# Kernel tuning notes

Hardware: AMD Instinct MI355X
Metric: run time of the kernel (lower is better)

The kernel has to match this reference:

```python
import jax, jax.numpy as jnp
import numpy as np

B, L, D_MODEL, D_STATE, D_CONV, EXPAND = 2, 1024, 1024, 16, 4, 2
D_INNER = D_MODEL * EXPAND


def setup_inputs() -> dict:
    key = jax.random.key(0)
    ks = jax.random.split(key, 8)
    s = lambda fan: 1.0 / np.sqrt(fan)
    x = jax.random.normal(ks[0], (B, L, D_MODEL), jnp.float32)
    in_proj_w = jax.random.normal(ks[1], (D_MODEL, 2 * D_INNER), jnp.float32) * s(D_MODEL)
    conv_w = jax.random.normal(ks[2], (D_INNER, 1, D_CONV), jnp.float32) * s(D_CONV)
    conv_b = jax.random.normal(ks[3], (D_INNER,), jnp.float32) * 0.01
    x_proj_w = jax.random.normal(ks[4], (D_INNER, 2 * D_STATE + D_INNER), jnp.float32) * s(D_INNER)
    dt_proj_w = jax.random.normal(ks[5], (D_INNER, D_INNER), jnp.float32) * s(D_INNER)
    dt_proj_b = jax.random.normal(ks[6], (D_INNER,), jnp.float32) * 0.01
    A_log = jnp.log(jnp.tile(jnp.arange(1, D_STATE + 1, dtype=jnp.float32)[None, :], (D_INNER, 1)))
    D = jnp.ones((D_INNER,), jnp.float32)
    out_proj_w = jax.random.normal(ks[7], (D_INNER, D_MODEL), jnp.float32) * s(D_INNER)
    return {"x": x, "in_proj_w": in_proj_w, "conv_w": conv_w, "conv_b": conv_b,
            "x_proj_w": x_proj_w, "dt_proj_w": dt_proj_w, "dt_proj_b": dt_proj_b,
            "A_log": A_log, "D": D, "out_proj_w": out_proj_w}


def _mamba_forward(x, in_proj_w, conv_w, conv_b, x_proj_w, dt_proj_w, dt_proj_b, A_log, D, out_proj_w):
    Bb, Ll, _ = x.shape
    d_inner, _, d_conv = conv_w.shape
    d_state = A_log.shape[1]
    # input projection and gate split
    xz = x @ in_proj_w                       # [B, L, 2*Di]
    x_inner, z = jnp.split(xz, 2, axis=-1)   # each [B, L, Di]
    # causal depthwise conv (left pad k-1, truncate to L == torch pad+slice)
    xc = jnp.transpose(x_inner, (0, 2, 1))   # [B, Di, L]
    xc = jax.lax.conv_general_dilated(
        xc, conv_w, window_strides=(1,), padding=[(d_conv - 1, 0)],
        dimension_numbers=("NCH", "OIH", "NCH"), feature_group_count=d_inner)
    xc = xc + conv_b[None, :, None]
    u = jax.nn.silu(jnp.transpose(xc, (0, 2, 1)))  # [B, L, Di]
    # SSM parameter projections
    ssm = u @ x_proj_w                        # [B, L, 2N+Di]
    B_ssm = ssm[..., :d_state]                # [B, L, N]
    C_ssm = ssm[..., d_state:2 * d_state]     # [B, L, N]
    dt = jax.nn.softplus(ssm[..., 2 * d_state:] @ dt_proj_w + dt_proj_b)  # [B, L, Di]
    A_real = -jnp.exp(A_log)                  # [Di, N]
    # selective scan over sequence (recurrence via lax.scan)
    def step(h, inp):
        dt_t, B_t, u_t = inp                  # [B,Di], [B,N], [B,Di]
        dA = jnp.exp(dt_t[..., None] * A_real)            # [B, Di, N]
        dBu = dt_t[..., None] * B_t[:, None, :] * u_t[..., None]
        h = dA * h + dBu
        return h, h
    h0 = jnp.zeros((Bb, d_inner, d_state), x.dtype)
    xs = (jnp.swapaxes(dt, 0, 1), jnp.swapaxes(B_ssm, 0, 1), jnp.swapaxes(u, 0, 1))
    _, states = jax.lax.scan(step, h0, xs)    # [L, B, Di, N]
    y = jnp.einsum("lbdn,lbn->lbd", states, jnp.swapaxes(C_ssm, 0, 1))
    y = jnp.swapaxes(y, 0, 1) + D * u         # skip connection
    y = y * jax.nn.silu(z)                    # gating
    return y @ out_proj_w                     # [B, L, d_model]


def reference(x, in_proj_w, conv_w, conv_b, x_proj_w, dt_proj_w, dt_proj_b, A_log, D, out_proj_w):
    return _mamba_forward(x, in_proj_w, conv_w, conv_b, x_proj_w, dt_proj_w, dt_proj_b, A_log, D, out_proj_w)
```

## Files before the change

kernel.cpp:

```cpp
#include <hip/hip_runtime.h>
#include <hip/hip_bf16.h>

#define BB 2
#define LL 1024
#define DMODEL 1024
#define DINNER 2048
#define DSTATE 16
#define DCONV 4
#define MM (BB * LL)
#define N_XZ 4096
#define N_SSM 2080
#define N_SSM_PAD 2176
#define CCH 32
#define LCH 32

typedef __hip_bfloat16 bf16;
typedef short bf16x8 __attribute__((ext_vector_type(8)));
typedef float f32x4 __attribute__((ext_vector_type(4)));

__device__ __forceinline__ void load16_lds(const bf16* g, bf16* l) {
    __builtin_amdgcn_global_load_lds(
        (const __attribute__((address_space(1))) void*)g,
        (__attribute__((address_space(3))) void*)l,
        16, 0, 0);
}

__global__ __launch_bounds__(256) void prep_kernel(
    const float* __restrict__ x, bf16* __restrict__ xbf,
    const float* __restrict__ w1, bf16* __restrict__ o1,
    const float* __restrict__ w2, bf16* __restrict__ o2,
    const float* __restrict__ w3, bf16* __restrict__ o3,
    const float* __restrict__ w4, bf16* __restrict__ o4)
{
    int bid = blockIdx.x;
    const float* src; bf16* dst; int K, N, tn, tk;
    if (bid < 4096)        { src = w1; dst = o1; K = 1024; N = 4096; tn = bid & 127; tk = bid >> 7; }
    else if (bid < 8256)   { bid -= 4096;  src = w2; dst = o2; K = 2048; N = 2080; tn = bid % 65; tk = bid / 65; }
    else if (bid < 12352)  { bid -= 8256;  src = w3; dst = o3; K = 2048; N = 2048; tn = bid & 63; tk = bid >> 6; }
    else if (bid < 14400)  { bid -= 12352; src = w4; dst = o4; K = 2048; N = 1024; tn = bid & 31; tk = bid >> 5; }
    else {
        bid -= 14400;
        int i = (bid * 256 + threadIdx.x) * 4;
        float4 v = *(const float4*)(x + i);
        xbf[i + 0] = __float2bfloat16(v.x);
        xbf[i + 1] = __float2bfloat16(v.y);
        xbf[i + 2] = __float2bfloat16(v.z);
        xbf[i + 3] = __float2bfloat16(v.w);
        return;
    }
    __shared__ float tile[32][33];
    const int nb = tn * 32, kb = tk * 32;
    const int tx = threadIdx.x & 31, ty = threadIdx.x >> 5;
    #pragma unroll
    for (int i = 0; i < 32; i += 8) {
        int k = kb + ty + i, n = nb + tx;
        tile[ty + i][tx] = (k < K && n < N) ? src[(size_t)k * N + n] : 0.f;
    }
    __syncthreads();
    #pragma unroll
    for (int i = 0; i < 32; i += 8) {
        int n = nb + ty + i, k = kb + tx;
        if (n < N && k < K) dst[(size_t)n * K + k] = __float2bfloat16(tile[tx][ty + i]);
    }
}

#define TM 128
#define TN 64
#define TK 64
template<int EPI, int KSPLIT = 1>
__global__ __launch_bounds__(256) void mfma_gemm(
    const bf16* __restrict__ A, int lda,
    const bf16* __restrict__ Wt, int ldw,
    float* __restrict__ Cf, bf16* __restrict__ Cb, int ldc,
    const float* __restrict__ bias,
    int N, int K)
{
    __shared__ __align__(16) bf16 As[TM * TK];
    __shared__ __align__(16) bf16 Bs[TN * TK];
    const int tid = threadIdx.x;
    const int wave = tid >> 6, lane = tid & 63;
    const int wm = (wave >> 1) * 64, wn = (wave & 1) * 32;
    const int m0 = blockIdx.y * TM, n0 = blockIdx.x * TN;
    const int lm = lane & 15, kq = lane >> 4;

    const int srow = lane >> 3;
    const int schunk = (lane & 7) ^ srow;
    const bf16* gA = A + (size_t)(m0 + wave * 32 + srow) * lda + schunk * 8;
    const bf16* gB = Wt + (size_t)(n0 + wave * 16 + srow) * ldw + schunk * 8;
    bf16* lA = &As[(wave * 32) * TK];
    bf16* lB = &Bs[(wave * 16) * TK];

    const int Kc = K / KSPLIT;
    const int kbeg = (KSPLIT > 1) ? blockIdx.z * Kc : 0;

    f32x4 acc[4][2] = {};
    const int fsw = (lm & 7);

    for (int it = 0; it < Kc; it += TK) {
        const int k0 = kbeg + it;
        #pragma unroll
        for (int g = 0; g < 4; ++g)
            load16_lds(gA + (size_t)(8 * g) * lda + k0, lA + (8 * g) * TK);
        #pragma unroll
        for (int g = 0; g < 2; ++g)
            load16_lds(gB + (size_t)(8 * g) * ldw + k0, lB + (8 * g) * TK);
        __syncthreads();

        bf16x8 af[4][2], bfr[2][2];
        #pragma unroll
        for (int i = 0; i < 4; ++i)
            #pragma unroll
            for (int t = 0; t < 2; ++t)
                af[i][t] = *(const bf16x8*)(&As[(wm + i * 16 + lm) * TK + ((t * 4 + kq) ^ fsw) * 8]);
        #pragma unroll
        for (int j = 0; j < 2; ++j)
            #pragma unroll
            for (int t = 0; t < 2; ++t)
                bfr[j][t] = *(const bf16x8*)(&Bs[(wn + j * 16 + lm) * TK + ((t * 4 + kq) ^ fsw) * 8]);
        #pragma unroll
        for (int t = 0; t < 2; ++t)
            #pragma unroll
            for (int i = 0; i < 4; ++i)
                #pragma unroll
                for (int j = 0; j < 2; ++j)
                    acc[i][j] = __builtin_amdgcn_mfma_f32_16x16x32_bf16(af[i][t], bfr[j][t], acc[i][j], 0, 0, 0);
        __syncthreads();
    }

    #pragma unroll
    for (int i = 0; i < 4; ++i) {
        #pragma unroll
        for (int j = 0; j < 2; ++j) {
            int gcol = n0 + wn + j * 16 + lm;
            if ((EPI == 0 || EPI == 3) && gcol >= N) continue;
            #pragma unroll
            for (int r = 0; r < 4; ++r) {
                int grow = m0 + wm + i * 16 + kq * 4 + r;
                float v = acc[i][j][r];
                if (EPI == 1) {
                    v += bias[gcol];
                    v = (v > 20.f) ? v : log1pf(__expf(v));
                    Cf[(size_t)grow * ldc + gcol] = v;
                } else if (EPI == 2) {
                    if (KSPLIT > 1) atomicAdd(&Cf[(size_t)grow * ldc + gcol], v);
                    else            Cf[(size_t)grow * ldc + gcol] = v;
                } else if (EPI == 3) {
                    if (gcol < 32) Cf[(size_t)grow * 32 + gcol] = v;
                    else           Cb[(size_t)grow * ldc + gcol] = __float2bfloat16(v);
                } else {
                    Cb[(size_t)grow * ldc + gcol] = __float2bfloat16(v);
                }
            }
        }
    }
}

__global__ void conv_silu_kernel(const bf16* __restrict__ xz,
                                 const float* __restrict__ conv_w,
                                 const float* __restrict__ conv_b,
                                 bf16* __restrict__ u)
{
    int idx = blockIdx.x * blockDim.x + threadIdx.x;
    if (idx >= BB * LL * DINNER) return;
    int d = idx & (DINNER - 1);
    int l = (idx >> 11) & (LL - 1);
    int b = idx >> 21;
    float acc = conv_b[d];
    #pragma unroll
    for (int j = 0; j < DCONV; ++j) {
        int ll = l - (DCONV - 1) + j;
        if (ll >= 0) {
            float xv = (float)xz[((size_t)(b * LL + ll)) * N_XZ + d];
            acc = fmaf(conv_w[d * DCONV + j], xv, acc);
        }
    }
    u[idx] = __float2bfloat16(acc / (1.f + __expf(-acc)));
}

__global__ __launch_bounds__(256) void scan_phase_a(
    const float* __restrict__ dt, const bf16* __restrict__ u,
    const float* __restrict__ BC,
    const float* __restrict__ A_log,
    float* __restrict__ chunkP, float* __restrict__ chunkH)
{
    const int d = blockIdx.x * 256 + threadIdx.x;
    const int c = blockIdx.y, b = blockIdx.z;
    const int l0 = c * LCH;

    float A[DSTATE];
    {
        const f32x4* ap = (const f32x4*)(A_log + d * DSTATE);
        #pragma unroll
        for (int q = 0; q < 4; ++q) {
            f32x4 v = ap[q];
            #pragma unroll
            for (int r = 0; r < 4; ++r) A[q * 4 + r] = -__expf(v[r]);
        }
    }
    float h[DSTATE];
    #pragma unroll
    for (int n = 0; n < DSTATE; ++n) h[n] = 0.f;
    float sdt = 0.f;

    const float* dtp = dt + ((size_t)b * LL + l0) * DINNER + d;
    const bf16* up = u + ((size_t)b * LL + l0) * DINNER + d;
    const float* bcp = BC + ((size_t)b * LL + l0) * 32;

    #pragma unroll 2
    for (int i = 0; i < LCH; ++i) {
        float dtv = *dtp;
        float uv  = (float)*up;
        float du  = dtv * uv;
        f32x4 Bv[4];
        #pragma unroll
        for (int q = 0; q < 4; ++q) Bv[q] = *(const f32x4*)(bcp + q * 4);
        #pragma unroll
        for (int n = 0; n < DSTATE; ++n) {
            float a = __expf(dtv * A[n]);
            h[n] = fmaf(a, h[n], du * Bv[n >> 2][n & 3]);
        }
        sdt += dtv;
        dtp += DINNER; up += DINNER; bcp += 32;
    }

    size_t idx = (((size_t)b * CCH + c) * DINNER + d) * DSTATE;
    #pragma unroll
    for (int q = 0; q < 4; ++q) {
        f32x4 pv, hv;
        #pragma unroll
        for (int r = 0; r < 4; ++r) { pv[r] = __expf(A[q * 4 + r] * sdt); hv[r] = h[q * 4 + r]; }
        *(f32x4*)(chunkP + idx + q * 4) = pv;
        *(f32x4*)(chunkH + idx + q * 4) = hv;
    }
}

__global__ __launch_bounds__(256) void scan_phase_p(
    const float* __restrict__ chunkP, float* __restrict__ chunkH)
{
    int gid = blockIdx.x * 256 + threadIdx.x;
    int n = gid & 15;
    int d = (gid >> 4) & (DINNER - 1);
    int b = gid >> 15;
    const size_t stride = (size_t)DINNER * DSTATE;
    size_t idx = ((size_t)b * CCH * DINNER + d) * DSTATE + n;
    float H = 0.f;
    for (int c = 0; c < CCH; ++c) {
        float P  = chunkP[idx];
        float hl = chunkH[idx];
        chunkH[idx] = H;
        H = fmaf(P, H, hl);
        idx += stride;
    }
}

__global__ __launch_bounds__(256) void scan_phase_b(
    const float* __restrict__ dt, bf16* __restrict__ u,
    const float* __restrict__ BC, const bf16* __restrict__ xz,
    const float* __restrict__ A_log, const float* __restrict__ Dp,
    const float* __restrict__ chunkH)
{
    const int d = blockIdx.x * 256 + threadIdx.x;
    const int c = blockIdx.y, b = blockIdx.z;
    const int l0 = c * LCH;

    float A[DSTATE];
    {
        const f32x4* ap = (const f32x4*)(A_log + d * DSTATE);
        #pragma unroll
        for (int q = 0; q < 4; ++q) {
            f32x4 v = ap[q];
            #pragma unroll
            for (int r = 0; r < 4; ++r) A[q * 4 + r] = -__expf(v[r]);
        }
    }
    const float Dd = Dp[d];
    float h[DSTATE];
    {
        size_t idx = (((size_t)b * CCH + c) * DINNER + d) * DSTATE;
        #pragma unroll
        for (int q = 0; q < 4; ++q) {
            f32x4 v = *(const f32x4*)(chunkH + idx + q * 4);
            #pragma unroll
            for (int r = 0; r < 4; ++r) h[q * 4 + r] = v[r];
        }
    }

    const float* dtp = dt + ((size_t)b * LL + l0) * DINNER + d;
    bf16* up = u + ((size_t)b * LL + l0) * DINNER + d;
    const float* bcp = BC + ((size_t)b * LL + l0) * 32;
    const bf16* zp = xz + ((size_t)b * LL + l0) * N_XZ + DINNER + d;

    #pragma unroll 2
    for (int i = 0; i < LCH; ++i) {
        float dtv = *dtp;
        float uv  = (float)*up;
        float du  = dtv * uv;
        f32x4 Bv[4], Cv[4];
        #pragma unroll
        for (int q = 0; q < 4; ++q) {
            Bv[q] = *(const f32x4*)(bcp + q * 4);
            Cv[q] = *(const f32x4*)(bcp + 16 + q * 4);
        }
        float acc = 0.f;
        #pragma unroll
        for (int n = 0; n < DSTATE; ++n) {
            float a = __expf(dtv * A[n]);
            h[n] = fmaf(a, h[n], du * Bv[n >> 2][n & 3]);
            acc = fmaf(h[n], Cv[n >> 2][n & 3], acc);
        }
        float zv = (float)*zp;
        acc = fmaf(Dd, uv, acc);
        acc *= zv / (1.f + __expf(-zv));
        *up = __float2bfloat16(acc);
        dtp += DINNER; up += DINNER; bcp += 32; zp += N_XZ;
    }
}

extern "C" void kernel_launch(void* const* d_in, const int* in_sizes, int n_in,
                              void* d_out, int out_size, void* d_ws, size_t ws_size,
                              hipStream_t stream) {
    const float* x         = (const float*)d_in[0];
    const float* in_proj_w = (const float*)d_in[1];
    const float* conv_w    = (const float*)d_in[2];
    const float* conv_b    = (const float*)d_in[3];
    const float* x_proj_w  = (const float*)d_in[4];
    const float* dt_proj_w = (const float*)d_in[5];
    const float* dt_proj_b = (const float*)d_in[6];
    const float* A_log     = (const float*)d_in[7];
    const float* Dp        = (const float*)d_in[8];
    const float* out_proj_w= (const float*)d_in[9];
    float* out = (float*)d_out;

    char* p = (char*)d_ws;
    float* dt   = (float*)p;                          p += (size_t)MM * DINNER * 4;
    bf16*  xbf  = (bf16*)dt;
    bf16*  xz   = (bf16*)p;                           p += (size_t)MM * N_XZ * 2;
    bf16*  u    = (bf16*)p;                           p += (size_t)MM * DINNER * 2;
    bf16*  ssm  = (bf16*)p;                           p += (size_t)MM * N_SSM * 2;
    bf16*  Wt1  = (bf16*)p;                           p += (size_t)N_XZ * DMODEL * 2;
    bf16*  Wt2  = (bf16*)p;                           p += (size_t)N_SSM_PAD * DINNER * 2;
    bf16*  Wt3  = (bf16*)p;                           p += (size_t)DINNER * DINNER * 2;
    bf16*  Wt4  = (bf16*)p;                           p += (size_t)DMODEL * DINNER * 2;
    float* BC   = (float*)p;                          p += (size_t)MM * 32 * 4;
    float* chunkP = (float*)Wt1;
    float* chunkH = (float*)Wt2;

    prep_kernel<<<16448, 256, 0, stream>>>(x, xbf, in_proj_w, Wt1, x_proj_w, Wt2,
                                           dt_proj_w, Wt3, out_proj_w, Wt4);
    mfma_gemm<0><<<dim3(N_XZ / TN, MM / TM), 256, 0, stream>>>(
        xbf, DMODEL, Wt1, DMODEL, nullptr, xz, N_XZ, nullptr, N_XZ, DMODEL);
    {
        int n = BB * LL * DINNER;
        conv_silu_kernel<<<(n + 255) / 256, 256, 0, stream>>>(xz, conv_w, conv_b, u);
    }
    mfma_gemm<3><<<dim3(N_SSM_PAD / TN, MM / TM), 256, 0, stream>>>(
        u, DINNER, Wt2, DINNER, BC, ssm, N_SSM, nullptr, N_SSM, DINNER);
    mfma_gemm<1><<<dim3(DINNER / TN, MM / TM), 256, 0, stream>>>(
        ssm + 2 * DSTATE, N_SSM, Wt3, DINNER, dt, nullptr, DINNER, dt_proj_b, DINNER, DINNER);
    scan_phase_a<<<dim3(DINNER / 256, CCH, BB), 256, 0, stream>>>(dt, u, BC, A_log, chunkP, chunkH);
    scan_phase_p<<<dim3(BB * DINNER * DSTATE / 256), 256, 0, stream>>>(chunkP, chunkH);
    scan_phase_b<<<dim3(DINNER / 256, CCH, BB), 256, 0, stream>>>(dt, u, BC, xz, A_log, Dp, chunkH);
    hipMemsetAsync(out, 0, (size_t)out_size * sizeof(float), stream);
    mfma_gemm<2, 2><<<dim3(DMODEL / TN, MM / TM, 2), 256, 0, stream>>>(
        u, DINNER, Wt4, DINNER, out, nullptr, DMODEL, nullptr, DMODEL, DINNER);
}
```

Before: 340.0 us.

## Double-buffer GEMM LDS tiles and add XCD-aware block swizzle

Gives the MFMA GEMM two LDS buffers so global-to-LDS loads for the next K tile are issued while the current tile is computed, using explicit waitcnt and barrier instructions in place of __syncthreads. It also adds an optional block-index remap that groups neighbouring N tiles onto the same XCD, aiming for better L2 reuse of the weight and activation tiles. LDS use doubles, which may lower occupancy. The hand-coded waitcnt masks and the loop that consumes two K tiles per iteration assume an even tile count.

```diff
diff --git a/kernel.cpp b/kernel.cpp
--- a/kernel.cpp
+++ b/kernel.cpp
@@ -67,7 +67,7 @@
 #define TM 128
 #define TN 64
 #define TK 64
-template<int EPI, int KSPLIT = 1>
+template<int EPI, int KSPLIT = 1, int SWZ = -1>
 __global__ __launch_bounds__(256) void mfma_gemm(
     const bf16* __restrict__ A, int lda,
     const bf16* __restrict__ Wt, int ldw,
@@ -75,48 +75,57 @@
     const float* __restrict__ bias,
     int N, int K)
 {
-    __shared__ __align__(16) bf16 As[TM * TK];
-    __shared__ __align__(16) bf16 Bs[TN * TK];
+    __shared__ __align__(16) bf16 As[2][TM * TK];
+    __shared__ __align__(16) bf16 Bs[2][TN * TK];
     const int tid = threadIdx.x;
     const int wave = tid >> 6, lane = tid & 63;
     const int wm = (wave >> 1) * 64, wn = (wave & 1) * 32;
-    const int m0 = blockIdx.y * TM, n0 = blockIdx.x * TN;
+
+    int bx, by;
+    if (SWZ >= 0) {
+        int id = blockIdx.x + (int)(gridDim.x * blockIdx.y);
+        int xcd = id & 7, slot = id >> 3;
+        bx = (xcd << SWZ) + (slot & ((1 << SWZ) - 1));
+        by = slot >> SWZ;
+    } else { bx = blockIdx.x; by = blockIdx.y; }
+    const int m0 = by * TM, n0 = bx * TN;
     const int lm = lane & 15, kq = lane >> 4;
 
     const int srow = lane >> 3;
     const int schunk = (lane & 7) ^ srow;
     const bf16* gA = A + (size_t)(m0 + wave * 32 + srow) * lda + schunk * 8;
     const bf16* gB = Wt + (size_t)(n0 + wave * 16 + srow) * ldw + schunk * 8;
-    bf16* lA = &As[(wave * 32) * TK];
-    bf16* lB = &Bs[(wave * 16) * TK];
 
     const int Kc = K / KSPLIT;
     const int kbeg = (KSPLIT > 1) ? blockIdx.z * Kc : 0;
+    const int NK = Kc / TK;
 
     f32x4 acc[4][2] = {};
     const int fsw = (lm & 7);
 
-    for (int it = 0; it < Kc; it += TK) {
-        const int k0 = kbeg + it;
+    auto stage = [&](int buf, int it) {
+        const int k0 = kbeg + it * TK;
+        bf16* lA = &As[buf][(wave * 32) * TK];
+        bf16* lB = &Bs[buf][(wave * 16) * TK];
         #pragma unroll
         for (int g = 0; g < 4; ++g)
             load16_lds(gA + (size_t)(8 * g) * lda + k0, lA + (8 * g) * TK);
         #pragma unroll
         for (int g = 0; g < 2; ++g)
             load16_lds(gB + (size_t)(8 * g) * ldw + k0, lB + (8 * g) * TK);
-        __syncthreads();
-
+    };
+    auto compute = [&](int buf) {
         bf16x8 af[4][2], bfr[2][2];
         #pragma unroll
         for (int i = 0; i < 4; ++i)
             #pragma unroll
             for (int t = 0; t < 2; ++t)
-                af[i][t] = *(const bf16x8*)(&As[(wm + i * 16 + lm) * TK + ((t * 4 + kq) ^ fsw) * 8]);
+                af[i][t] = *(const bf16x8*)(&As[buf][(wm + i * 16 + lm) * TK + ((t * 4 + kq) ^ fsw) * 8]);
         #pragma unroll
         for (int j = 0; j < 2; ++j)
             #pragma unroll
             for (int t = 0; t < 2; ++t)
-                bfr[j][t] = *(const bf16x8*)(&Bs[(wn + j * 16 + lm) * TK + ((t * 4 + kq) ^ fsw) * 8]);
+                bfr[j][t] = *(const bf16x8*)(&Bs[buf][(wn + j * 16 + lm) * TK + ((t * 4 + kq) ^ fsw) * 8]);
         #pragma unroll
         for (int t = 0; t < 2; ++t)
             #pragma unroll
@@ -124,7 +133,24 @@
                 #pragma unroll
                 for (int j = 0; j < 2; ++j)
                     acc[i][j] = __builtin_amdgcn_mfma_f32_16x16x32_bf16(af[i][t], bfr[j][t], acc[i][j], 0, 0, 0);
-        __syncthreads();
+    };
+
+    stage(0, 0);
+    for (int it = 0; it < NK; it += 2) {
+        stage(1, it + 1);
+        __builtin_amdgcn_s_waitcnt(0x0F76);
+        __builtin_amdgcn_s_barrier();
+        compute(0);
+        __builtin_amdgcn_s_barrier();
+        if (it + 2 < NK) {
+            stage(0, it + 2);
+            __builtin_amdgcn_s_waitcnt(0x0F76);
+        } else {
+            __builtin_amdgcn_s_waitcnt(0x0F70);
+        }
+        __builtin_amdgcn_s_barrier();
+        compute(1);
+        __builtin_amdgcn_s_barrier();
     }
 
     #pragma unroll
@@ -347,7 +373,7 @@
 
     prep_kernel<<<16448, 256, 0, stream>>>(x, xbf, in_proj_w, Wt1, x_proj_w, Wt2,
                                            dt_proj_w, Wt3, out_proj_w, Wt4);
-    mfma_gemm<0><<<dim3(N_XZ / TN, MM / TM), 256, 0, stream>>>(
+    mfma_gemm<0, 1, 3><<<dim3(N_XZ / TN, MM / TM), 256, 0, stream>>>(
         xbf, DMODEL, Wt1, DMODEL, nullptr, xz, N_XZ, nullptr, N_XZ, DMODEL);
     {
         int n = BB * LL * DINNER;
@@ -355,12 +381,12 @@
     }
     mfma_gemm<3><<<dim3(N_SSM_PAD / TN, MM / TM), 256, 0, stream>>>(
         u, DINNER, Wt2, DINNER, BC, ssm, N_SSM, nullptr, N_SSM, DINNER);
-    mfma_gemm<1><<<dim3(DINNER / TN, MM / TM), 256, 0, stream>>>(
+    mfma_gemm<1, 1, 2><<<dim3(DINNER / TN, MM / TM), 256, 0, stream>>>(
         ssm + 2 * DSTATE, N_SSM, Wt3, DINNER, dt, nullptr, DINNER, dt_proj_b, DINNER, DINNER);
     scan_phase_a<<<dim3(DINNER / 256, CCH, BB), 256, 0, stream>>>(dt, u, BC, A_log, chunkP, chunkH);
     scan_phase_p<<<dim3(BB * DINNER * DSTATE / 256), 256, 0, stream>>>(chunkP, chunkH);
     scan_phase_b<<<dim3(DINNER / 256, CCH, BB), 256, 0, stream>>>(dt, u, BC, xz, A_log, Dp, chunkH);
     hipMemsetAsync(out, 0, (size_t)out_size * sizeof(float), stream);
-    mfma_gemm<2, 2><<<dim3(DMODEL / TN, MM / TM, 2), 256, 0, stream>>>(
+    mfma_gemm<2, 2, 1><<<dim3(DMODEL / TN, MM / TM, 2), 256, 0, stream>>>(
         u, DINNER, Wt4, DINNER, out, nullptr, DMODEL, nullptr, DMODEL, DINNER);
 }
```

Result: faster. 333.1 us (-2.0%).
